# Optimization experiments

Hardware: AMD Instinct MI355X
Metric: run time of the kernel (lower is better)

## Reference

```python
import jax, jax.numpy as jnp
import numpy as np

NEG = -1000000000.0  # mask value used by the original module

def setup_inputs() -> dict:
    key = jax.random.key(0)
    kq, kk, kv, kl = jax.random.split(key, 4)
    B, Lq, Lk, D, Dv = 16, 2048, 2048, 64, 64
    q = jax.random.normal(kq, (B, Lq, D), dtype=jnp.float32)
    k = jax.random.normal(kk, (B, Lk, D), dtype=jnp.float32)
    v = jax.random.normal(kv, (B, Lk, Dv), dtype=jnp.float32)
    valid_len = jax.random.randint(kl, (B, Lq), 0, Lk, dtype=jnp.int32)
    return {"q": q, "k": k, "v": v, "valid_len": valid_len}

def reference(q, k, v, valid_len):
    # scores: [B, Lq, Lk]  (NOTE: original module does NOT scale by sqrt(d))
    scores = jnp.einsum('bqd,bkd->bqk', q, k)
    Lk = k.shape[1]
    # per-(batch,query) valid length masking over the key dimension
    mask = jnp.arange(Lk, dtype=valid_len.dtype)[None, None, :] < valid_len[:, :, None]
    scores = jnp.where(mask, scores, NEG)
    attn = jax.nn.softmax(scores, axis=-1)
    # dropout p=0.0 -> identity
    return jnp.einsum('bqk,bkv->bqv', attn, v)
```

## Files before the change

kernel.cpp:

```cpp
#include <hip/hip_runtime.h>

typedef _Float16 f16;
typedef __attribute__((ext_vector_type(8))) _Float16 f16x8;
typedef __attribute__((ext_vector_type(4))) _Float16 f16x4;
typedef __attribute__((ext_vector_type(4))) float f32x4;

#define NB 16
#define LSEQ 2048
#define DIM 64
#define KVB 64
#define QT 128
#define NQT (LSEQ / QT)
#define NT (LSEQ / KVB)
#define LOG2E 1.44269504088896340736f

__device__ inline f16x4 pkcvt(const f32x4 x) {
    auto a = __builtin_amdgcn_cvt_pkrtz(x[0], x[1]);
    auto b = __builtin_amdgcn_cvt_pkrtz(x[2], x[3]);
    f16x4 t; t[0]=(f16)a[0]; t[1]=(f16)a[1]; t[2]=(f16)b[0]; t[3]=(f16)b[1];
    return t;
}

__device__ inline void gload16(const void* g, void* l) {
    __builtin_amdgcn_global_load_lds(
        (const __attribute__((address_space(1))) unsigned int*)g,
        (__attribute__((address_space(3))) unsigned int*)l, 16, 0, 0);
}

__device__ __host__ inline int kappa(int p) {
    int kt = p >> 4, hi = (p >> 2) & 3, g = p & 3;
    return ((kt & 1) << 5) + (hi << 3) + ((kt >> 1) << 2) + g;
}

__global__ __launch_bounds__(256) void prep(
    const float* __restrict__ kg, const float* __restrict__ vg,
    const int* __restrict__ vlg,
    f16* __restrict__ k16, f16* __restrict__ v16, int* __restrict__ perm)
{
    const int tid = threadIdx.x;
    if (blockIdx.x < NB * NT) {
        const int b = blockIdx.x & 15, t = blockIdx.x >> 4;
        const int bt = b * NT + t;
        const float* kb_ = kg + ((size_t)b * LSEQ + t * KVB) * DIM;
        const float* vb_ = vg + ((size_t)b * LSEQ + t * KVB) * DIM;
        f16* kd = k16 + (size_t)bt * (KVB * DIM);
        f16* vd = v16 + (size_t)bt * (KVB * DIM);
#pragma unroll
        for (int it = 0; it < 4; ++it) {
            int cc = tid + it * 256;
            int row = cc >> 4, c4 = (cc & 15) * 4;
            f32x4 x = *(const f32x4*)(kb_ + kappa(row) * DIM + c4);
            *(f16x4*)(kd + row * 64 + (c4 ^ ((row & 7) * 8))) = pkcvt(x);
        }
        int kb4 = tid & 15, dvb = tid >> 4;
        f32x4 rr[4];
#pragma unroll
        for (int i = 0; i < 4; ++i)
            rr[i] = *(const f32x4*)(vb_ + (size_t)(kb4 * 4 + i) * DIM + dvb * 4);
#pragma unroll
        for (int j = 0; j < 4; ++j) {
            int dv = dvb * 4 + j;
            f32x4 col = {rr[0][j], rr[1][j], rr[2][j], rr[3][j]};
            *(f16x4*)(vd + dv * 64 + ((kb4 * 4) ^ ((dv & 7) * 8))) = pkcvt(col);
        }
    } else {
        const int b = blockIdx.x - NB * NT;
        __shared__ int hist[NT + 1];
        __shared__ int base[NT + 1];
        if (tid <= NT) hist[tid] = 0;
        __syncthreads();
        for (int q = tid; q < LSEQ; q += 256) {
            int vl = vlg[b * LSEQ + q];
            int t = (vl == 0) ? NT : ((vl + KVB - 1) >> 6);
            atomicAdd(&hist[t], 1);
        }
        __syncthreads();
        if (tid == 0) {
            int acc = 0;
            for (int t = NT; t >= 0; --t) { base[t] = acc; acc += hist[t]; }
        }
        __syncthreads();
        for (int q = tid; q < LSEQ; q += 256) {
            int vl = vlg[b * LSEQ + q];
            int t = (vl == 0) ? NT : ((vl + KVB - 1) >> 6);
            int pos = atomicAdd(&base[t], 1);
            perm[b * LSEQ + pos] = q;
        }
    }
}

__global__ __launch_bounds__(256, 4) void attn_fwd(
    const float* __restrict__ qg, const int* __restrict__ vlg,
    const f16* __restrict__ k16, const f16* __restrict__ v16,
    float* __restrict__ outg, const int* __restrict__ perm,
    f16* __restrict__ opart, float* __restrict__ mlg, int S)
{
    __shared__ alignas(16) f16 kbuf[2][KVB * 64];
    __shared__ alignas(16) f16 vbuf[2][DIM * 64];
    __shared__ int wmax[4];

    const int tid  = threadIdx.x;
    const int wid  = tid >> 6;
    const int lane = tid & 63;
    const int r    = lane & 15;
    const int hi   = lane >> 4;

    const int bid = blockIdx.x;
    const int nbs = NB * S;
    const int qt  = bid / nbs;
    const int rem = bid - qt * nbs;
    const int s   = rem >> 4;
    const int b   = rem & 15;
    const int qw  = qt * QT + wid * 16;

    const int qidxA = perm[b * LSEQ + qw + r];
    const int qidxB = perm[b * LSEQ + qw + 64 + r];
    const int vlA   = vlg[b * LSEQ + qidxA];
    const int vlB   = vlg[b * LSEQ + qidxB];

    int tq = max((vlA == 0) ? NT : ((vlA + KVB - 1) >> 6),
                 (vlB == 0) ? NT : ((vlB + KVB - 1) >> 6));
    tq = max(tq, __shfl_xor(tq, 1));
    tq = max(tq, __shfl_xor(tq, 2));
    tq = max(tq, __shfl_xor(tq, 4));
    tq = max(tq, __shfl_xor(tq, 8));
    if (lane == 0) wmax[wid] = tq;
    __syncthreads();
    const int maxt = max(max(wmax[0], wmax[1]), max(wmax[2], wmax[3]));

    auto rmin = [&](int v) {
        v = min(v, __shfl_xor(v, 1));
        v = min(v, __shfl_xor(v, 2));
        v = min(v, __shfl_xor(v, 4));
        v = min(v, __shfl_xor(v, 8));
        return v;
    };
    const int vminA = rmin(vlA);
    const int vminB = rmin(vlB);

    auto load_q = [&](int qidx, f16x8* qf) {
        const float* qrow = qg + ((size_t)(b * LSEQ + qidx)) * DIM;
#pragma unroll
        for (int ks = 0; ks < 2; ++ks) {
            f32x4 x = *(const f32x4*)(qrow + ks * 32 + hi * 8);
            f32x4 y = *(const f32x4*)(qrow + ks * 32 + hi * 8 + 4);
            f32x4 xs = {x[0]*LOG2E, x[1]*LOG2E, x[2]*LOG2E, x[3]*LOG2E};
            f32x4 ys = {y[0]*LOG2E, y[1]*LOG2E, y[2]*LOG2E, y[3]*LOG2E};
            f16x4 lo = pkcvt(xs), hh = pkcvt(ys);
            f16x8 t;
            t[0]=lo[0]; t[1]=lo[1]; t[2]=lo[2]; t[3]=lo[3];
            t[4]=hh[0]; t[5]=hh[1]; t[6]=hh[2]; t[7]=hh[3];
            qf[ks] = t;
        }
    };
    f16x8 qfA[2], qfB[2];
    load_q(qidxA, qfA);
    load_q(qidxB, qfB);

    float mA = -INFINITY, mB = -INFINITY;
    float lA = 0.0f, lB = 0.0f;
    f32x4 oA[4], oB[4];
#pragma unroll
    for (int dt = 0; dt < 4; ++dt) { oA[dt] = f32x4{0,0,0,0}; oB[dt] = f32x4{0,0,0,0}; }

    const f16* kt_base = k16 + (size_t)b * (NT * KVB * DIM);
    const f16* vt_base = v16 + (size_t)b * (NT * KVB * DIM);
    const int swz = (r & 7) * 8;

    auto stage = [&](int bi, int t) {
        const char* ks = (const char*)(kt_base + (size_t)t * 4096);
        const char* vs = (const char*)(vt_base + (size_t)t * 4096);
        char* kd = (char*)&kbuf[bi][0];
        char* vd = (char*)&vbuf[bi][0];
        gload16(ks + tid * 16,        kd + tid * 16);
        gload16(ks + 4096 + tid * 16, kd + 4096 + tid * 16);
        gload16(vs + tid * 16,        vd + tid * 16);
        gload16(vs + 4096 + tid * 16, vd + 4096 + tid * 16);
    };

    auto do_frag = [&](const f16x8* qf, int vl, int vmin,
                       float& m_run, float& l_run, f32x4* o,
                       int kv0, const f16* kb_, const f16* vb_) {
        f32x4 st[4];
        __builtin_amdgcn_s_setprio(1);
#pragma unroll
        for (int kt = 0; kt < 4; ++kt) {
            f32x4 acc = f32x4{0,0,0,0};
#pragma unroll
            for (int ks = 0; ks < 2; ++ks) {
                f16x8 kf = *(const f16x8*)(&kb_[(kt * 16 + r) * 64 + ((ks * 32 + hi * 8) ^ swz)]);
                acc = __builtin_amdgcn_mfma_f32_16x16x32_f16(kf, qf[ks], acc, 0, 0, 0);
            }
            st[kt] = acc;
        }
        __builtin_amdgcn_s_setprio(0);

        float lanemax = -INFINITY;
        if (kv0 + KVB > vmin) {
#pragma unroll
            for (int kt = 0; kt < 4; ++kt)
#pragma unroll
                for (int g = 0; g < 4; ++g) {
                    int key = kv0 + ((kt & 1) << 5) + (hi << 3) + ((kt >> 1) << 2) + g;
                    float sv = (key < vl) ? st[kt][g] : -1e9f;
                    st[kt][g] = sv;
                    lanemax = fmaxf(lanemax, sv);
                }
        } else {
#pragma unroll
            for (int kt = 0; kt < 4; ++kt)
#pragma unroll
                for (int g = 0; g < 4; ++g)
                    lanemax = fmaxf(lanemax, st[kt][g]);
        }

        if (__any(lanemax > m_run + 8.0f)) {
            float tmax = lanemax;
            tmax = fmaxf(tmax, __shfl_xor(tmax, 16));
            tmax = fmaxf(tmax, __shfl_xor(tmax, 32));
            float m_new = fmaxf(m_run, tmax);
            float scale = exp2f(m_run - m_new);
            l_run *= scale;
            m_run = m_new;
#pragma unroll
            for (int g = 0; g < 4; ++g) {
                float sc = __shfl(scale, hi * 4 + g);
#pragma unroll
                for (int dt = 0; dt < 4; ++dt) o[dt][g] *= sc;
            }
        }

        f16x8 pa[2];
#pragma unroll
        for (int kt = 0; kt < 4; ++kt)
#pragma unroll
            for (int g = 0; g < 4; ++g) {
                float p = exp2f(st[kt][g] - m_run);
                l_run += p;
                pa[kt & 1][((kt >> 1) << 2) + g] = (f16)p;
            }

        __builtin_amdgcn_s_setprio(1);
#pragma unroll
        for (int ks = 0; ks < 2; ++ks)
#pragma unroll
            for (int dt = 0; dt < 4; ++dt) {
                f16x8 vf = *(const f16x8*)(&vb_[(dt * 16 + r) * 64 + ((ks * 32 + hi * 8) ^ swz)]);
                o[dt] = __builtin_amdgcn_mfma_f32_16x16x32_f16(pa[ks], vf, o[dt], 0, 0, 0);
            }
        __builtin_amdgcn_s_setprio(0);
    };

    if (s < maxt) stage(0, s);
    int c = 0;
    for (int tt = s; tt < maxt; tt += S) {
        __syncthreads();
        if (tt + S < maxt) stage(c ^ 1, tt + S);
        const int kv0 = tt * KVB;
        do_frag(qfA, vlA, vminA, mA, lA, oA, kv0, &kbuf[c][0], &vbuf[c][0]);
        do_frag(qfB, vlB, vminB, mB, lB, oB, kv0, &kbuf[c][0], &vbuf[c][0]);
        c ^= 1;
    }

    auto epi = [&](float m_run, float l_run, f32x4* o, int qidx) {
        l_run += __shfl_xor(l_run, 16);
        l_run += __shfl_xor(l_run, 32);
        if (S == 1) {
            float inv = 1.0f / l_run;
#pragma unroll
            for (int g = 0; g < 4; ++g) {
                float iv = __shfl(inv, hi * 4 + g);
                int   qo = __shfl(qidx, hi * 4 + g);
                float* ob = outg + ((size_t)(b * LSEQ + qo)) * DIM;
#pragma unroll
                for (int dt = 0; dt < 4; ++dt)
                    ob[dt * 16 + r] = o[dt][g] * iv;
            }
        } else {
            f16* obase = opart + ((size_t)s * NB * LSEQ + (size_t)b * LSEQ) * DIM;
#pragma unroll
            for (int g = 0; g < 4; ++g) {
                int qo = __shfl(qidx, hi * 4 + g);
                f16* ob = obase + (size_t)qo * DIM;
#pragma unroll
                for (int dt = 0; dt < 4; ++dt)
                    ob[dt * 16 + r] = (f16)o[dt][g];
            }
            if (hi == 0) {
                size_t mi = ((size_t)s * NB * LSEQ + (size_t)b * LSEQ + qidx) * 2;
                mlg[mi]     = m_run;
                mlg[mi + 1] = l_run;
            }
        }
    };
    epi(mA, lA, oA, qidxA);
    epi(mB, lB, oB, qidxB);
}

__global__ void merge_k(const f16* __restrict__ opart, const float* __restrict__ mlg,
                        float* __restrict__ outg, int S)
{
    const int gt = blockIdx.x * 256 + threadIdx.x;
    const size_t base = (size_t)gt * 4;
    const size_t qg = base >> 6;
    float M = -INFINITY;
    for (int s = 0; s < S; ++s)
        M = fmaxf(M, mlg[((size_t)s * NB * LSEQ + qg) * 2]);
    float den = 0.f;
    f32x4 acc = {0.f, 0.f, 0.f, 0.f};
    for (int s = 0; s < S; ++s) {
        size_t mi = ((size_t)s * NB * LSEQ + qg) * 2;
        float w = exp2f(mlg[mi] - M);
        den += w * mlg[mi + 1];
        f16x4 ov = *(const f16x4*)(opart + (size_t)s * (NB * LSEQ * DIM) + base);
        acc[0] += w * (float)ov[0]; acc[1] += w * (float)ov[1];
        acc[2] += w * (float)ov[2]; acc[3] += w * (float)ov[3];
    }
    float inv = 1.0f / den;
    f32x4 res = {acc[0]*inv, acc[1]*inv, acc[2]*inv, acc[3]*inv};
    *(f32x4*)(outg + base) = res;
}

extern "C" void kernel_launch(void* const* d_in, const int* in_sizes, int n_in,
                              void* d_out, int out_size, void* d_ws, size_t ws_size,
                              hipStream_t stream) {
    const float* q  = (const float*)d_in[0];
    const float* k  = (const float*)d_in[1];
    const float* v  = (const float*)d_in[2];
    const int*   vl = (const int*)d_in[3];
    float* out = (float*)d_out;

    const size_t perm_b = (size_t)NB * LSEQ * sizeof(int);
    const size_t kv_b   = (size_t)NB * LSEQ * DIM * sizeof(f16);
    auto need = [&](int S) {
        return perm_b + 2 * kv_b
             + (size_t)S * NB * LSEQ * 2 * sizeof(float)
             + (size_t)S * NB * LSEQ * DIM * sizeof(f16);
    };
    int S;
    if      (ws_size >= need(4)) S = 4;
    else if (ws_size >= need(2)) S = 2;
    else                         S = 1;

    int*   perm  = (int*)d_ws;
    f16*   k16   = (f16*)((char*)d_ws + perm_b);
    f16*   v16   = (f16*)((char*)d_ws + perm_b + kv_b);
    float* mlg   = (float*)((char*)d_ws + perm_b + 2 * kv_b);
    f16*   opart = (f16*)((char*)d_ws + perm_b + 2 * kv_b
                          + (size_t)S * NB * LSEQ * 2 * sizeof(float));

    prep<<<NB * NT + NB, 256, 0, stream>>>(k, v, vl, k16, v16, perm);

    attn_fwd<<<dim3(NQT * NB * S), dim3(256), 0, stream>>>(
        q, vl, k16, v16, out, perm, opart, mlg, S);

    if (S > 1) {
        const int mthreads = NB * LSEQ * DIM / 4;
        merge_k<<<dim3(mthreads / 256), dim3(256), 0, stream>>>(opart, mlg, out, S);
    }
}
```

Before: 46.17 us.

## Interleave the two query fragments to share K/V LDS fragment loads

Restructures the per-tile inner loop so both query fragments (A and B) are processed together. Each K and V fragment is read from LDS once and fed to MFMAs for both fragments, rather than being loaded separately per fragment, and the two fragments' MFMAs interleave to hide dependency latency. This halves LDS reads for K/V and gives the scheduler more independent MFMA chains, at the cost of more live registers (two score sets and two probability sets at once), which may hurt occupancy.

Result: no change. 46.03 us (median of 2 runs) (-0.3%).

```diff
diff --git a/kernel.cpp b/kernel.cpp
--- a/kernel.cpp
+++ b/kernel.cpp
@@ -178,23 +178,8 @@
         gload16(vs + 4096 + tid * 16, vd + 4096 + tid * 16);
     };
 
-    auto do_frag = [&](const f16x8* qf, int vl, int vmin,
-                       float& m_run, float& l_run, f32x4* o,
-                       int kv0, const f16* kb_, const f16* vb_) {
-        f32x4 st[4];
-        __builtin_amdgcn_s_setprio(1);
-#pragma unroll
-        for (int kt = 0; kt < 4; ++kt) {
-            f32x4 acc = f32x4{0,0,0,0};
-#pragma unroll
-            for (int ks = 0; ks < 2; ++ks) {
-                f16x8 kf = *(const f16x8*)(&kb_[(kt * 16 + r) * 64 + ((ks * 32 + hi * 8) ^ swz)]);
-                acc = __builtin_amdgcn_mfma_f32_16x16x32_f16(kf, qf[ks], acc, 0, 0, 0);
-            }
-            st[kt] = acc;
-        }
-        __builtin_amdgcn_s_setprio(0);
-
+    auto do_sm = [&](f32x4* st, int vl, int vmin, float& m_run, float& l_run,
+                     f32x4* o, int kv0, f16x8* pa) {
         float lanemax = -INFINITY;
         if (kv0 + KVB > vmin) {
 #pragma unroll
@@ -230,7 +215,6 @@
             }
         }
 
-        f16x8 pa[2];
 #pragma unroll
         for (int kt = 0; kt < 4; ++kt)
 #pragma unroll
@@ -239,16 +223,6 @@
                 l_run += p;
                 pa[kt & 1][((kt >> 1) << 2) + g] = (f16)p;
             }
-
-        __builtin_amdgcn_s_setprio(1);
-#pragma unroll
-        for (int ks = 0; ks < 2; ++ks)
-#pragma unroll
-            for (int dt = 0; dt < 4; ++dt) {
-                f16x8 vf = *(const f16x8*)(&vb_[(dt * 16 + r) * 64 + ((ks * 32 + hi * 8) ^ swz)]);
-                o[dt] = __builtin_amdgcn_mfma_f32_16x16x32_f16(pa[ks], vf, o[dt], 0, 0, 0);
-            }
-        __builtin_amdgcn_s_setprio(0);
     };
 
     if (s < maxt) stage(0, s);
@@ -257,8 +231,34 @@
         __syncthreads();
         if (tt + S < maxt) stage(c ^ 1, tt + S);
         const int kv0 = tt * KVB;
-        do_frag(qfA, vlA, vminA, mA, lA, oA, kv0, &kbuf[c][0], &vbuf[c][0]);
-        do_frag(qfB, vlB, vminB, mB, lB, oB, kv0, &kbuf[c][0], &vbuf[c][0]);
+
+        f32x4 stA[4], stB[4];
+        __builtin_amdgcn_s_setprio(1);
+#pragma unroll
+        for (int kt = 0; kt < 4; ++kt) {
+            f16x8 kf0 = *(const f16x8*)(&kbuf[c][(kt * 16 + r) * 64 + ((0 * 32 + hi * 8) ^ swz)]);
+            f16x8 kf1 = *(const f16x8*)(&kbuf[c][(kt * 16 + r) * 64 + ((1 * 32 + hi * 8) ^ swz)]);
+            f32x4 a = __builtin_amdgcn_mfma_f32_16x16x32_f16(kf0, qfA[0], f32x4{0,0,0,0}, 0, 0, 0);
+            stA[kt] = __builtin_amdgcn_mfma_f32_16x16x32_f16(kf1, qfA[1], a, 0, 0, 0);
+            f32x4 bb = __builtin_amdgcn_mfma_f32_16x16x32_f16(kf0, qfB[0], f32x4{0,0,0,0}, 0, 0, 0);
+            stB[kt] = __builtin_amdgcn_mfma_f32_16x16x32_f16(kf1, qfB[1], bb, 0, 0, 0);
+        }
+        __builtin_amdgcn_s_setprio(0);
+
+        f16x8 paA[2], paB[2];
+        do_sm(stA, vlA, vminA, mA, lA, oA, kv0, paA);
+        do_sm(stB, vlB, vminB, mB, lB, oB, kv0, paB);
+
+        __builtin_amdgcn_s_setprio(1);
+#pragma unroll
+        for (int dt = 0; dt < 4; ++dt)
+#pragma unroll
+            for (int ks = 0; ks < 2; ++ks) {
+                f16x8 vf = *(const f16x8*)(&vbuf[c][(dt * 16 + r) * 64 + ((ks * 32 + hi * 8) ^ swz)]);
+                oA[dt] = __builtin_amdgcn_mfma_f32_16x16x32_f16(paA[ks], vf, oA[dt], 0, 0, 0);
+                oB[dt] = __builtin_amdgcn_mfma_f32_16x16x32_f16(paB[ks], vf, oB[dt], 0, 0, 0);
+            }
+        __builtin_amdgcn_s_setprio(0);
         c ^= 1;
     }
 
```
